# Performance work log

Measured on AMD Instinct MI355X. Metric: run time of the kernel, lower is better.

Reference implementation:

```python
import jax, jax.numpy as jnp
import numpy as np
from jax import lax
from jax.scipy.special import erf

SB, NV, NR = 2, 3, 2048
NC, NS, NG = 1000, 40, 15
H = W = 256
HID = 256
DEPTH_DIFF_MAX = 0.05
IMG = jnp.array([float(W), float(H)], dtype=jnp.float32)


def setup_inputs():
    key = jax.random.key(0)
    ks = jax.random.split(key, 10)
    origins = 0.1 * jax.random.normal(ks[0], (SB, NR, 3), jnp.float32)
    d_xy = 0.3 * jax.random.normal(ks[1], (SB, NR, 2), jnp.float32)
    dirs = jnp.concatenate([d_xy, jnp.ones((SB, NR, 1), jnp.float32)], -1)
    dirs = dirs / jnp.linalg.norm(dirs, axis=-1, keepdims=True)
    near = jnp.ones((SB, NR, 1), jnp.float32)
    far = 4.0 * jnp.ones((SB, NR, 1), jnp.float32)
    rays = jnp.concatenate([origins, dirs, near, far], -1)
    pose = jnp.eye(4, dtype=jnp.float32).at[2, 3].set(0.5)
    poses = jnp.broadcast_to(pose, (SB, NV, 4, 4))
    focal = 280.0 * jnp.ones((SB, NV, 2), jnp.float32)
    c = 128.0 * jnp.ones((SB, NV, 2), jnp.float32)
    depth_map = 1.5 + 3.0 * jax.random.uniform(ks[2], (SB, NV, 1, H, W), jnp.float32)
    depth_std_map = 0.01 + 0.2 * jax.random.uniform(ks[3], (SB, NV, 1, H, W), jnp.float32)
    nrm = jax.random.normal(ks[4], (SB, NV, 3, H, W), jnp.float32)
    normal_map = nrm / jnp.linalg.norm(nrm, axis=2, keepdims=True)
    W1 = 0.5 * jax.random.normal(ks[5], (6, HID), jnp.float32)
    b1 = jnp.zeros((HID,), jnp.float32)
    W2 = 0.1 * jax.random.normal(ks[6], (HID, 4), jnp.float32)
    b2 = jnp.zeros((4,), jnp.float32)
    u_coarse = jax.random.uniform(ks[7], (SB, NR, NC), jnp.float32)
    g_noise = jax.random.normal(ks[8], (SB, NR, NG), jnp.float32)
    u_fill = jax.random.uniform(ks[9], (SB, NR, NS), jnp.float32)
    return dict(rays=rays, poses=poses, focal=focal, c=c, depth_map=depth_map,
                depth_std_map=depth_std_map, normal_map=normal_map,
                W1=W1, b1=b1, W2=W2, b2=b2,
                u_coarse=u_coarse, g_noise=g_noise, u_fill=u_fill)


def _index_map(feat, uv):
    # feat: (SB,NV,C,H,W), uv: (SB,NV,P,2) in [-1,1] -> (SB,NV,C,P), nearest lookup
    sb, nv, ch, h, w = feat.shape
    x = jnp.clip(jnp.round((uv[..., 0] + 1) * 0.5 * w - 0.5), 0, w - 1).astype(jnp.int32)
    y = jnp.clip(jnp.round((uv[..., 1] + 1) * 0.5 * h - 0.5), 0, h - 1).astype(jnp.int32)
    lin = y * w + x
    flat = feat.reshape(sb, nv, ch, h * w)
    idx = jnp.broadcast_to(lin[:, :, None, :], (sb, nv, ch, lin.shape[-1]))
    return jnp.take_along_axis(flat, idx, axis=-1)


def _sample_z(rays, poses, focal, c, depth_map, depth_std_map, normal_map, u_coarse, g_noise, u_fill):
    near, far = rays[..., 6], rays[..., 7]
    step = 1.0 / NC
    # stratified coarse candidates (SB,NR,NC)
    z_steps = jnp.linspace(0.0, 1.0 - step, NC, dtype=jnp.float32)[None, None, :] + u_coarse * step
    z_cand = near[..., None] * (1 - z_steps) + far[..., None] * z_steps
    P = NR * NC
    xyz_w = (rays[..., None, :3] + z_cand[..., None] * rays[..., None, 3:6]).reshape(SB, P, 3)
    R, t = poses[:, :, :3, :3], poses[:, :, :3, 3]
    xyz = jnp.einsum('svij,spj->svpi', R, xyz_w) + t[:, :, None, :]   # (SB,NV,P,3) cam coords
    rdir_cam = jnp.einsum('svij,srj->svri', R, rays[..., 3:6])        # (SB,NV,NR,3)
    pdir_cam = jnp.repeat(rdir_cam, NC, axis=2)                        # (SB,NV,P,3)
    uv = xyz[..., :2] / xyz[..., 2:3]
    uv = (uv * focal[:, :, None, :] + c[:, :, None, :]) / IMG * 2 - 1
    ref_depth = _index_map(depth_map, uv)                              # (SB,NV,1,P)
    ref_std = _index_map(depth_std_map, uv)
    ref_normal = _index_map(normal_map, uv)                            # (SB,NV,3,P)
    ref_z = xyz[..., 2][:, :, None, :]                                 # (SB,NV,1,P)
    ss = jnp.repeat((far - near) / NC, NC, axis=1)[:, None, None, :]   # (SB,1,1,P)
    cosd = jnp.sum(jnp.swapaxes(pdir_cam, -2, -1) * ref_normal, axis=-2, keepdims=True)
    mask = (ref_std != 0) & (jnp.abs(ref_depth - ref_z) < DEPTH_DIFF_MAX) & (cosd <= 0)
    inv = 1.0 / (jnp.where(mask, ref_std, 1.0) * jnp.sqrt(2.0))
    lik = 0.5 * jnp.abs(erf((ref_z + ss / 2 - ref_depth) * inv) - erf((ref_z - ss / 2 - ref_depth) * inv))
    pt = jnp.where(mask, lik, 0.0)
    pt = jnp.max(pt, axis=1)[:, 0, :].reshape(SB, NR, NC)              # max over views
    opaque = jnp.concatenate(
        [pt[..., :1], pt[..., 1:] * jnp.cumprod(1.0 - pt, axis=-1)[..., :-1]], -1)
    sel_lik, idx = lax.top_k(pt, NS)                                   # descending shortlist
    z_sel = jnp.take_along_axis(z_cand, idx, axis=-1)
    z_sel = jnp.where(sel_lik == 0.0, 0.0, z_sel)
    # gaussian samples fitted to occlusion-aware likelihoods
    ray_mask = jnp.any(opaque != 0.0, axis=-1)                         # (SB,NR)
    wsum = jnp.sum(opaque, -1, keepdims=True)
    sw = jnp.where(wsum > 0, wsum, 1.0)
    mean = jnp.sum(z_cand * opaque, -1, keepdims=True) / sw
    std = jnp.sqrt(jnp.sum(opaque * (z_cand - mean) ** 2, -1, keepdims=True) / sw)
    gauss = jnp.where(ray_mask[..., None], g_noise * std + mean, 0.0)
    z_sel = z_sel.at[..., NS - NG:].set(gauss)
    # fill empty slots (zeros, which sort to the front) uniformly in [near, far]
    z = jnp.sort(z_sel, axis=-1)
    miss = z == 0.0
    n_miss = jnp.sum(miss, -1, keepdims=True)
    stepf = (far - near)[..., None] / jnp.maximum(n_miss, 1)
    z_fill = near[..., None] + jnp.arange(NS, dtype=jnp.float32)[None, None, :] * stepf + u_fill * stepf
    z = jnp.where(miss, z_fill, z)
    return jnp.sort(z, axis=-1)                                        # (SB,NR,NS)


def _composite(rays, z, W1, b1, W2, b2):
    deltas = jnp.concatenate([z[..., 1:] - z[..., :-1], rays[..., 7:8] - z[..., -1:]], -1)
    pts = rays[..., None, :3] + z[..., None] * rays[..., None, 3:6]    # (SB,NR,NS,3)
    dirs = jnp.broadcast_to(rays[..., None, 3:6], pts.shape)
    h = jax.nn.relu(jnp.concatenate([pts, dirs], -1) @ W1 + b1)        # NeRF surrogate MLP
    out = h @ W2 + b2                                                  # (SB,NR,NS,4)
    rgbs, sig = out[..., :3], out[..., 3]
    alphas = 1.0 - jnp.exp(-deltas * jax.nn.relu(sig))
    T = jnp.cumprod(jnp.concatenate([jnp.ones_like(alphas[..., :1]), 1.0 - alphas + 1e-10], -1), -1)
    weights = alphas * T[..., :-1]
    rgb = jnp.sum(weights[..., None] * rgbs, -2)
    depth = jnp.sum(weights * z, -1)
    rgb = rgb + 1.0 - jnp.sum(weights, -1, keepdims=True)              # white background
    return weights, rgb, depth


def reference(rays, poses, focal, c, depth_map, depth_std_map, normal_map, W1, b1, W2, b2, u_coarse, g_noise, u_fill):
    # depth-guided sampling is under @torch.no_grad in the original -> stop_gradient
    z = lax.stop_gradient(_sample_z(rays, poses, focal, c, depth_map, depth_std_map,
                                    normal_map, u_coarse, g_noise, u_fill))
    return _composite(rays, z, W1, b1, W2, b2)
```

## Files before the change

kernel.cpp:

```cpp
#include <hip/hip_runtime.h>
#include <math.h>

#define N_SB 2
#define N_V  3
#define N_R  2048
#define N_C  1000
#define N_S  40
#define N_G  15
#define N_HID 256
#define HW 65536
#define CAP 256

__device__ __forceinline__ float wave_sum(float v) {
#pragma unroll
  for (int off = 32; off > 0; off >>= 1) v += __shfl_xor(v, off);
  return v;
}

__device__ __forceinline__ float erf_xla(float x) {
  const float c = 3.832506856900711f;
  x = fminf(fmaxf(x, -c), c);
  float x2 = __fmul_rn(x, x);
  float p = 0.00022905065861350646f;
  p = __fadd_rn(__fmul_rn(p, x2), 0.0034082910107109506f);
  p = __fadd_rn(__fmul_rn(p, x2), 0.050955695062380861f);
  p = __fadd_rn(__fmul_rn(p, x2), 0.18520832239976145f);
  p = __fadd_rn(__fmul_rn(p, x2), 1.128379143519084f);
  float q = -1.1791602954361697e-7f;
  q = __fadd_rn(__fmul_rn(q, x2), 0.000023547966471313185f);
  q = __fadd_rn(__fmul_rn(q, x2), 0.0010179625278914885f);
  q = __fadd_rn(__fmul_rn(q, x2), 0.014070470171167667f);
  q = __fadd_rn(__fmul_rn(q, x2), 0.11098505178285362f);
  q = __fadd_rn(__fmul_rn(q, x2), 0.49746925110067538f);
  q = __fadd_rn(__fmul_rn(q, x2), 1.0f);
  return __fdiv_rn(__fmul_rn(x, p), q);
}

__device__ __forceinline__ float bitonic64(float v, int lane) {
#pragma unroll
  for (int k = 2; k <= 64; k <<= 1) {
#pragma unroll
    for (int j = k >> 1; j >= 1; j >>= 1) {
      float o = __shfl_xor(v, j);
      bool up = ((lane & k) == 0);
      bool lower = ((lane & j) == 0);
      v = (lower == up) ? fminf(v, o) : fmaxf(v, o);
    }
  }
  return v;
}

__global__ __launch_bounds__(256, 8)
void nerf_all(const float* __restrict__ rays, const float* __restrict__ poses,
              const float* __restrict__ focal, const float* __restrict__ cvec,
              const float* __restrict__ dmap, const float* __restrict__ smap,
              const float* __restrict__ nmap, const float* __restrict__ W1,
              const float* __restrict__ b1, const float* __restrict__ W2,
              const float* __restrict__ b2, const float* __restrict__ uc,
              const float* __restrict__ gn, const float* __restrict__ uf,
              float* __restrict__ out)
{
  __shared__ __align__(16) float s_pt[1024];
  __shared__ __align__(16) float s_zc[1024];
  __shared__ float s_lv[CAP];
  __shared__ int   s_li[CAP];
  __shared__ float s_lz[CAP];
  __shared__ int   s_cnt;
  __shared__ float s_cv[100];
  __shared__ int   s_ci[100];
  __shared__ float s_cz[100];
  __shared__ float s_zsel[32];
  __shared__ float s_wtot[4], s_sO[4], s_sZ[4], s_sV[4];
  __shared__ int   s_fl[4];
  __shared__ float s_zarr[N_S], s_darr[N_S];
  __shared__ float s_mlp[N_S * 4];

  const int tid = threadIdx.x;
  const int wid = tid >> 6;
  const int lane = tid & 63;
  const int ray = blockIdx.x;
  const int sb = ray >> 11;

  if (tid == 0) s_cnt = 0;
  if (tid < 100) { s_cv[tid] = 0.0f; s_ci[tid] = 0x40000000; s_cz[tid] = 0.0f; }
  if (tid < 32) s_zsel[tid] = 0.0f;

  const float* rp = rays + (size_t)ray * 8;
  const float ox = rp[0], oy = rp[1], oz = rp[2];
  const float dx = rp[3], dy = rp[4], dz = rp[5];
  const float nearv = rp[6], farv = rp[7];

  const float lindelta = 0.999f / 999.0f;
  const float ssv = __fdiv_rn(__fsub_rn(farv, nearv), 1000.0f);
  const float sshalf = __fmul_rn(ssv, 0.5f);
  const float SQRT2 = 1.41421356237309515f;

  float zg[4] = {0.0f, 0.0f, 0.0f, 0.0f};
  float ptg[4] = {0.0f, 0.0f, 0.0f, 0.0f};
#pragma unroll
  for (int cch = 0; cch < 4; ++cch) {
    const int i = cch * 256 + tid;
    if (i < N_C) {
      const float u = uc[(size_t)ray * N_C + i];
      const float zs = __fadd_rn(__fmul_rn((float)i, lindelta), __fmul_rn(u, 0.001f));
      const float zc = __fadd_rn(__fmul_rn(nearv, __fsub_rn(1.0f, zs)), __fmul_rn(farv, zs));
      zg[cch] = zc;
      s_zc[i] = zc;
    }
  }

#pragma unroll 1
  for (int v = 0; v < N_V; ++v) {
    const float* pp = poses + (size_t)(sb * N_V + v) * 16;
    const float R00 = pp[0], R01 = pp[1], R02 = pp[2], t0 = pp[3];
    const float R10 = pp[4], R11 = pp[5], R12 = pp[6], t1 = pp[7];
    const float R20 = pp[8], R21 = pp[9], R22 = pp[10], t2 = pp[11];
    const float fx = focal[(sb * N_V + v) * 2 + 0];
    const float fy = focal[(sb * N_V + v) * 2 + 1];
    const float cx = cvec[(sb * N_V + v) * 2 + 0];
    const float cy = cvec[(sb * N_V + v) * 2 + 1];
    const float rdx = __fadd_rn(__fadd_rn(__fmul_rn(R00, dx), __fmul_rn(R01, dy)), __fmul_rn(R02, dz));
    const float rdy = __fadd_rn(__fadd_rn(__fmul_rn(R10, dx), __fmul_rn(R11, dy)), __fmul_rn(R12, dz));
    const float rdz = __fadd_rn(__fadd_rn(__fmul_rn(R20, dx), __fmul_rn(R21, dy)), __fmul_rn(R22, dz));
    const float* dmv = dmap + (size_t)(sb * N_V + v) * HW;
    const float* smv = smap + (size_t)(sb * N_V + v) * HW;
    const float* nmv = nmap + (size_t)(sb * N_V + v) * 3 * HW;

    int   linv[4];
    float Zcv[4];
    float rdv[4];
#pragma unroll
    for (int cch = 0; cch < 4; ++cch) {
      const float zc = zg[cch];
      const float xw = __fadd_rn(ox, __fmul_rn(zc, dx));
      const float yw = __fadd_rn(oy, __fmul_rn(zc, dy));
      const float zw = __fadd_rn(oz, __fmul_rn(zc, dz));
      const float Xc = __fadd_rn(__fadd_rn(__fadd_rn(__fmul_rn(R00, xw), __fmul_rn(R01, yw)), __fmul_rn(R02, zw)), t0);
      const float Yc = __fadd_rn(__fadd_rn(__fadd_rn(__fmul_rn(R10, xw), __fmul_rn(R11, yw)), __fmul_rn(R12, zw)), t1);
      const float Zc = __fadd_rn(__fadd_rn(__fadd_rn(__fmul_rn(R20, xw), __fmul_rn(R21, yw)), __fmul_rn(R22, zw)), t2);
      const float iu = __fdiv_rn(Xc, Zc);
      const float iv = __fdiv_rn(Yc, Zc);
      const float su = __fadd_rn(__fmul_rn(iu, fx), cx);
      const float sv = __fadd_rn(__fmul_rn(iv, fy), cy);
      const float unorm = __fsub_rn(__fmul_rn(__fmul_rn(su, 1.0f / 256.0f), 2.0f), 1.0f);
      const float vnorm = __fsub_rn(__fmul_rn(__fmul_rn(sv, 1.0f / 256.0f), 2.0f), 1.0f);
      const float xf = __fsub_rn(__fmul_rn(__fmul_rn(__fadd_rn(unorm, 1.0f), 0.5f), 256.0f), 0.5f);
      const float yf = __fsub_rn(__fmul_rn(__fmul_rn(__fadd_rn(vnorm, 1.0f), 0.5f), 256.0f), 0.5f);
      const int px = (int)fminf(fmaxf(rintf(xf), 0.0f), 255.0f);
      const int py = (int)fminf(fmaxf(rintf(yf), 0.0f), 255.0f);
      linv[cch] = py * 256 + px;
      Zcv[cch] = Zc;
      rdv[cch] = dmv[linv[cch]];
    }

#pragma unroll
    for (int cch = 0; cch < 4; ++cch) {
      const int i = cch * 256 + tid;
      const float Zc = Zcv[cch];
      const float rd = rdv[cch];
      if (i < N_C && fabsf(__fsub_rn(rd, Zc)) < 0.05f) {
        const int lin = linv[cch];
        const float rs = smv[lin];
        const float n0 = nmv[lin];
        const float n1 = nmv[HW + lin];
        const float n2 = nmv[2 * HW + lin];
        const float cosd = __fadd_rn(__fadd_rn(__fmul_rn(rdx, n0), __fmul_rn(rdy, n1)), __fmul_rn(rdz, n2));
        if ((rs != 0.0f) && (cosd <= 0.0f)) {
          const float invv = __fdiv_rn(1.0f, __fmul_rn(rs, SQRT2));
          const float a1 = __fmul_rn(__fsub_rn(__fadd_rn(Zc, sshalf), rd), invv);
          const float a2 = __fmul_rn(__fsub_rn(__fsub_rn(Zc, sshalf), rd), invv);
          const float ptv = __fmul_rn(0.5f, fabsf(__fsub_rn(erf_xla(a1), erf_xla(a2))));
          ptg[cch] = fmaxf(ptg[cch], ptv);
        }
      }
    }
  }
#pragma unroll
  for (int cch = 0; cch < 4; ++cch) {
    const int i = cch * 256 + tid;
    if (i < N_C) s_pt[i] = ptg[cch];
  }
  __syncthreads();

  const bool act = (tid < 250);
  float ptm[4] = {0.0f, 0.0f, 0.0f, 0.0f};
  float zcr[4] = {0.0f, 0.0f, 0.0f, 0.0f};
  if (act) {
    const float4 p4 = *(const float4*)&s_pt[tid * 4];
    ptm[0] = p4.x; ptm[1] = p4.y; ptm[2] = p4.z; ptm[3] = p4.w;
    const float4 z4 = *(const float4*)&s_zc[tid * 4];
    zcr[0] = z4.x; zcr[1] = z4.y; zcr[2] = z4.z; zcr[3] = z4.w;
  }

  float lp = 1.0f;
  if (act) {
#pragma unroll
    for (int k = 0; k < 4; ++k) lp = __fmul_rn(lp, __fsub_rn(1.0f, ptm[k]));
  }
  float inc = lp;
#pragma unroll
  for (int off = 1; off < 64; off <<= 1) {
    float o = __shfl_up(inc, off);
    if (lane >= off) inc *= o;
  }
  if (lane == 63) s_wtot[wid] = inc;
  __syncthreads();
  float pw = 1.0f;
  if (wid > 0) pw *= s_wtot[0];
  if (wid > 1) pw *= s_wtot[1];
  if (wid > 2) pw *= s_wtot[2];
  float exc = __shfl_up(inc, 1);
  if (lane == 0) exc = 1.0f;
  exc *= pw;

  float accO = 0.0f, accZO = 0.0f;
  bool anynz = false;
  if (act) {
    float run = exc;
#pragma unroll
    for (int k = 0; k < 4; ++k) {
      float o = ptm[k] * run;
      accO += o;
      accZO += zcr[k] * o;
      anynz |= (o != 0.0f);
      run *= (1.0f - ptm[k]);
    }
  }
  accO = wave_sum(accO);
  accZO = wave_sum(accZO);
  const int anyw = __any(anynz) ? 1 : 0;
  if (lane == 0) { s_sO[wid] = accO; s_sZ[wid] = accZO; s_fl[wid] = anyw; }
  __syncthreads();
  const float tO = s_sO[0] + s_sO[1] + s_sO[2] + s_sO[3];
  const float tZ = s_sZ[0] + s_sZ[1] + s_sZ[2] + s_sZ[3];
  const bool raymask = (s_fl[0] | s_fl[1] | s_fl[2] | s_fl[3]) != 0;
  const float swd = (tO > 0.0f) ? tO : 1.0f;
  const float meanz = __fdiv_rn(tZ, swd);

  float accV = 0.0f;
  if (act) {
    float run = exc;
#pragma unroll
    for (int k = 0; k < 4; ++k) {
      float o = ptm[k] * run;
      float d = zcr[k] - meanz;
      accV += o * d * d;
      run *= (1.0f - ptm[k]);
    }
  }
  accV = wave_sum(accV);
  if (lane == 0) s_sV[wid] = accV;
  __syncthreads();
  const float tV = s_sV[0] + s_sV[1] + s_sV[2] + s_sV[3];
  const float stdz = sqrtf(__fdiv_rn(tV, swd));

  {
    const bool nz0 = act && (ptm[0] > 0.0f);
    const bool nz1 = act && (ptm[1] > 0.0f);
    const bool nz2 = act && (ptm[2] > 0.0f);
    const bool nz3 = act && (ptm[3] > 0.0f);
    const int nloc = (int)nz0 + (int)nz1 + (int)nz2 + (int)nz3;
    int base = 0;
    if (nloc > 0) base = atomicAdd(&s_cnt, nloc);
    if (base + nloc <= CAP) {
      int off = base;
      if (nz0) { s_lv[off] = ptm[0]; s_li[off] = tid * 4 + 0; s_lz[off] = zcr[0]; ++off; }
      if (nz1) { s_lv[off] = ptm[1]; s_li[off] = tid * 4 + 1; s_lz[off] = zcr[1]; ++off; }
      if (nz2) { s_lv[off] = ptm[2]; s_li[off] = tid * 4 + 2; s_lz[off] = zcr[2]; ++off; }
      if (nz3) { s_lv[off] = ptm[3]; s_li[off] = tid * 4 + 3; s_lz[off] = zcr[3]; ++off; }
    }
  }
  __syncthreads();
  const int cnt = s_cnt;

  if (cnt <= CAP) {
    if (wid == 0) {
      float rv[4]; int ri[4]; float rz[4];
#pragma unroll
      for (int j = 0; j < 4; ++j) {
        const int p = lane + j * 64;
        if (p < cnt) { rv[j] = s_lv[p]; ri[j] = s_li[p]; rz[j] = s_lz[p]; }
        else         { rv[j] = -2.0f; ri[j] = 0x40000000; rz[j] = 0.0f; }
      }
#pragma unroll 1
      for (int kk = 0; kk < 25; ++kk) {
        float bv = -2.0f; int bi = 0x40000000;
#pragma unroll
        for (int j = 0; j < 4; ++j) {
          if (rv[j] > bv || (rv[j] == bv && ri[j] < bi)) { bv = rv[j]; bi = ri[j]; }
        }
#pragma unroll
        for (int off = 1; off < 64; off <<= 1) {
          const float ov = __shfl_xor(bv, off);
          const int oi = __shfl_xor(bi, off);
          if (ov > bv || (ov == bv && oi < bi)) { bv = ov; bi = oi; }
        }
        if (bv <= 0.0f) break;
#pragma unroll
        for (int j = 0; j < 4; ++j) {
          if (ri[j] == bi) {
            s_zsel[kk] = rz[j];
            rv[j] = -1.0f;
          }
        }
      }
    }
  } else {
    const int cbase = wid * 25;
#pragma unroll 1
    for (int kk = 0; kk < 25; ++kk) {
      float bv = -2.0f;
      int bi = 0x40000000;
      if (act) {
#pragma unroll
        for (int k = 0; k < 4; ++k) {
          if (ptm[k] > bv) { bv = ptm[k]; bi = tid * 4 + k; }
        }
      }
#pragma unroll
      for (int off = 1; off < 64; off <<= 1) {
        float ov = __shfl_xor(bv, off);
        int oi = __shfl_xor(bi, off);
        if (ov > bv || (ov == bv && oi < bi)) { bv = ov; bi = oi; }
      }
      if (bv <= 0.0f) break;
      if (tid == (bi >> 2)) {
        s_cv[cbase + kk] = bv;
        s_ci[cbase + kk] = bi;
        const int r = bi & 3;
        float zk;
        if (r == 0)      { zk = zcr[0]; ptm[0] = -1.0f; }
        else if (r == 1) { zk = zcr[1]; ptm[1] = -1.0f; }
        else if (r == 2) { zk = zcr[2]; ptm[2] = -1.0f; }
        else             { zk = zcr[3]; ptm[3] = -1.0f; }
        s_cz[cbase + kk] = zk;
      }
    }
    __syncthreads();
    if (wid == 0) {
      float c0v = s_cv[lane];
      int   c0i = s_ci[lane];
      float c0z = s_cz[lane];
      float c1v = -2.0f; int c1i = 0x40000000; float c1z = 0.0f;
      if (lane + 64 < 100) { c1v = s_cv[lane + 64]; c1i = s_ci[lane + 64]; c1z = s_cz[lane + 64]; }
#pragma unroll 1
      for (int kk = 0; kk < 25; ++kk) {
        float bv = c0v; int bi = c0i; float bz = c0z;
        if (c1v > bv || (c1v == bv && c1i < bi)) { bv = c1v; bi = c1i; bz = c1z; }
#pragma unroll
        for (int off = 1; off < 64; off <<= 1) {
          float ov = __shfl_xor(bv, off);
          int oi = __shfl_xor(bi, off);
          float oz = __shfl_xor(bz, off);
          if (ov > bv || (ov == bv && oi < bi)) { bv = ov; bi = oi; bz = oz; }
        }
        if (bv <= 0.0f) break;
        if (lane == 0) s_zsel[kk] = bz;
        if (c0i == bi) c0v = -1.0f;
        if (c1i == bi) c1v = -1.0f;
      }
    }
  }

  if (wid == 0) {
    float sortv;
    if (lane < N_S - N_G) {
      sortv = s_zsel[lane];
    } else if (lane < N_S) {
      const float g = gn[(size_t)ray * N_G + (lane - (N_S - N_G))];
      sortv = raymask ? (g * stdz + meanz) : 0.0f;
    } else {
      sortv = INFINITY;
    }
    float z = bitonic64(sortv, lane);
    const bool miss = (lane < N_S) && (z == 0.0f);
    const int nmiss_raw = __popcll(__ballot(miss));
    const int nmiss = (nmiss_raw < 1) ? 1 : nmiss_raw;
    const float stepf = __fdiv_rn(__fsub_rn(farv, nearv), (float)nmiss);
    if (miss) {
      const float ufv = uf[(size_t)ray * N_S + lane];
      z = __fadd_rn(__fadd_rn(nearv, __fmul_rn((float)lane, stepf)), __fmul_rn(ufv, stepf));
    }
    z = bitonic64(z, lane);
    const float zn = __shfl_down(z, 1);
    const float delta = (lane == N_S - 1) ? (farv - z) : (zn - z);
    if (lane < N_S) { s_zarr[lane] = z; s_darr[lane] = delta; }
  }
  __syncthreads();

  {
    const float b2r = (lane < 4) ? b2[lane] : 0.0f;
    float w1r[24], b1r[4], w2r[16];
#pragma unroll
    for (int m = 0; m < 4; ++m) {
      const int j = lane + 64 * m;
#pragma unroll
      for (int k = 0; k < 6; ++k) w1r[k * 4 + m] = W1[k * N_HID + j];
      b1r[m] = b1[j];
      const float4 w2v = *(const float4*)(W2 + (size_t)j * 4);
      w2r[m * 4 + 0] = w2v.x; w2r[m * 4 + 1] = w2v.y;
      w2r[m * 4 + 2] = w2v.z; w2r[m * 4 + 3] = w2v.w;
    }
#pragma unroll 1
    for (int q = 0; q < 10; ++q) {
      const int s = wid * 10 + q;
      const float zq = s_zarr[s];
      const float px = ox + zq * dx;
      const float py = oy + zq * dy;
      const float pz = oz + zq * dz;
      float a0 = 0.0f, a1 = 0.0f, a2 = 0.0f, a3 = 0.0f;
#pragma unroll
      for (int m = 0; m < 4; ++m) {
        float h = b1r[m];
        h = fmaf(px, w1r[0 * 4 + m], h);
        h = fmaf(py, w1r[1 * 4 + m], h);
        h = fmaf(pz, w1r[2 * 4 + m], h);
        h = fmaf(dx, w1r[3 * 4 + m], h);
        h = fmaf(dy, w1r[4 * 4 + m], h);
        h = fmaf(dz, w1r[5 * 4 + m], h);
        h = fmaxf(h, 0.0f);
        a0 = fmaf(h, w2r[m * 4 + 0], a0);
        a1 = fmaf(h, w2r[m * 4 + 1], a1);
        a2 = fmaf(h, w2r[m * 4 + 2], a2);
        a3 = fmaf(h, w2r[m * 4 + 3], a3);
      }
      const float s0 = __shfl_xor(a0, 1), s1 = __shfl_xor(a1, 1);
      const float s2 = __shfl_xor(a2, 1), s3 = __shfl_xor(a3, 1);
      const float m0 = (lane & 1) ? (a1 + s1) : (a0 + s0);
      const float m1 = (lane & 1) ? (a3 + s3) : (a2 + s2);
      const float t0 = __shfl_xor(m0, 2), t1 = __shfl_xor(m1, 2);
      float r = (lane & 2) ? (m1 + t1) : (m0 + t0);
#pragma unroll
      for (int off = 4; off < 64; off <<= 1) r += __shfl_xor(r, off);
      if (lane < 4) s_mlp[s * 4 + lane] = r + b2r;
    }
  }
  __syncthreads();

  if (wid == 0) {
    float alpha = 0.0f, r0 = 0.0f, r1 = 0.0f, r2 = 0.0f, zl = 0.0f;
    float factor = 1.0f;
    if (lane < N_S) {
      zl = s_zarr[lane];
      const float dl = s_darr[lane];
      r0 = s_mlp[lane * 4 + 0];
      r1 = s_mlp[lane * 4 + 1];
      r2 = s_mlp[lane * 4 + 2];
      const float rsig = fmaxf(s_mlp[lane * 4 + 3], 0.0f);
      alpha = 1.0f - expf(-dl * rsig);
      factor = (1.0f - alpha) + 1e-10f;
    }
    float incp = factor;
#pragma unroll
    for (int off = 1; off < 64; off <<= 1) {
      float o = __shfl_up(incp, off);
      if (lane >= off) incp *= o;
    }
    float T = __shfl_up(incp, 1);
    if (lane == 0) T = 1.0f;

    const float w = (lane < N_S) ? alpha * T : 0.0f;
    const float wz = (lane < N_S) ? w * zl : 0.0f;
    const float wr0 = (lane < N_S) ? w * r0 : 0.0f;
    const float wr1 = (lane < N_S) ? w * r1 : 0.0f;
    const float wr2 = (lane < N_S) ? w * r2 : 0.0f;

    const float wsum = wave_sum(w);
    const float dsum = wave_sum(wz);
    const float c0s = wave_sum(wr0);
    const float c1s = wave_sum(wr1);
    const float c2s = wave_sum(wr2);

    if (lane < N_S) out[(size_t)ray * N_S + lane] = w;
    if (lane == 0) {
      float* rgbo = out + (size_t)N_SB * N_R * N_S + (size_t)ray * 3;
      rgbo[0] = (c0s + 1.0f) - wsum;
      rgbo[1] = (c1s + 1.0f) - wsum;
      rgbo[2] = (c2s + 1.0f) - wsum;
      out[(size_t)N_SB * N_R * N_S + (size_t)N_SB * N_R * 3 + ray] = dsum;
    }
  }
}

extern "C" void kernel_launch(void* const* d_in, const int* in_sizes, int n_in,
                              void* d_out, int out_size, void* d_ws, size_t ws_size,
                              hipStream_t stream) {
  const float* rays  = (const float*)d_in[0];
  const float* poses = (const float*)d_in[1];
  const float* focal = (const float*)d_in[2];
  const float* cvec  = (const float*)d_in[3];
  const float* dmap  = (const float*)d_in[4];
  const float* smap  = (const float*)d_in[5];
  const float* nmap  = (const float*)d_in[6];
  const float* W1p   = (const float*)d_in[7];
  const float* b1p   = (const float*)d_in[8];
  const float* W2p   = (const float*)d_in[9];
  const float* b2p   = (const float*)d_in[10];
  const float* ucp   = (const float*)d_in[11];
  const float* gnp   = (const float*)d_in[12];
  const float* ufp   = (const float*)d_in[13];
  float* outp = (float*)d_out;

  dim3 grid(N_SB * N_R);
  dim3 block(256);
  nerf_all<<<grid, block, 0, stream>>>(rays, poses, focal, cvec, dmap, smap, nmap,
                                       W1p, b1p, W2p, b2p, ucp, gnp, ufp, outp);
}
```

Before: 96.59 us.

## Cut register pressure: union shared buffers, pair projections, split MLP hidden across waves

Several scattered shared arrays are merged into one aliased buffer, so the MLP partial sums reuse the space of dead sampling arrays. Coarse z values now live in LDS rather than registers, and the projection and gating run two samples at a time through helper functions. The MLP is reorganised so each thread owns one hidden unit across all 40 samples instead of four units for 10 samples. Per-wave partial results are reduced by wave 0 from LDS. The goal is to lower register and LDS footprint for higher occupancy, at the cost of extra LDS reads and a changed summation order.

Measured after the change: 141.3 us. +46.3%, slower.

```diff
diff --git a/kernel.cpp b/kernel.cpp
--- a/kernel.cpp
+++ b/kernel.cpp
@@ -7,7 +7,6 @@
 #define N_C  1000
 #define N_S  40
 #define N_G  15
-#define N_HID 256
 #define HW 65536
 #define CAP 256
 
@@ -50,6 +49,57 @@
   return v;
 }
 
+__device__ __forceinline__ void proj_one(
+    float zc, float ox, float oy, float oz, float dx, float dy, float dz,
+    float R00, float R01, float R02, float t0,
+    float R10, float R11, float R12, float t1,
+    float R20, float R21, float R22, float t2,
+    float fx, float fy, float cx, float cy,
+    int& lin_out, float& Zc_out)
+{
+  const float xw = __fadd_rn(ox, __fmul_rn(zc, dx));
+  const float yw = __fadd_rn(oy, __fmul_rn(zc, dy));
+  const float zw = __fadd_rn(oz, __fmul_rn(zc, dz));
+  const float Xc = __fadd_rn(__fadd_rn(__fadd_rn(__fmul_rn(R00, xw), __fmul_rn(R01, yw)), __fmul_rn(R02, zw)), t0);
+  const float Yc = __fadd_rn(__fadd_rn(__fadd_rn(__fmul_rn(R10, xw), __fmul_rn(R11, yw)), __fmul_rn(R12, zw)), t1);
+  const float Zc = __fadd_rn(__fadd_rn(__fadd_rn(__fmul_rn(R20, xw), __fmul_rn(R21, yw)), __fmul_rn(R22, zw)), t2);
+  const float iu = __fdiv_rn(Xc, Zc);
+  const float iv = __fdiv_rn(Yc, Zc);
+  const float su = __fadd_rn(__fmul_rn(iu, fx), cx);
+  const float sv = __fadd_rn(__fmul_rn(iv, fy), cy);
+  const float unorm = __fsub_rn(__fmul_rn(__fmul_rn(su, 1.0f / 256.0f), 2.0f), 1.0f);
+  const float vnorm = __fsub_rn(__fmul_rn(__fmul_rn(sv, 1.0f / 256.0f), 2.0f), 1.0f);
+  const float xf = __fsub_rn(__fmul_rn(__fmul_rn(__fadd_rn(unorm, 1.0f), 0.5f), 256.0f), 0.5f);
+  const float yf = __fsub_rn(__fmul_rn(__fmul_rn(__fadd_rn(vnorm, 1.0f), 0.5f), 256.0f), 0.5f);
+  const int px = (int)fminf(fmaxf(rintf(xf), 0.0f), 255.0f);
+  const int py = (int)fminf(fmaxf(rintf(yf), 0.0f), 255.0f);
+  lin_out = py * 256 + px;
+  Zc_out = Zc;
+}
+
+__device__ __forceinline__ float gate_one(
+    int i, int lin, float Zc, float rd,
+    const float* __restrict__ smv, const float* __restrict__ nmv,
+    float rdx, float rdy, float rdz, float sshalf, float cur)
+{
+  const float SQRT2 = 1.41421356237309515f;
+  if (i < N_C && fabsf(__fsub_rn(rd, Zc)) < 0.05f) {
+    const float rs = smv[lin];
+    const float n0 = nmv[lin];
+    const float n1 = nmv[HW + lin];
+    const float n2 = nmv[2 * HW + lin];
+    const float cosd = __fadd_rn(__fadd_rn(__fmul_rn(rdx, n0), __fmul_rn(rdy, n1)), __fmul_rn(rdz, n2));
+    if ((rs != 0.0f) && (cosd <= 0.0f)) {
+      const float invv = __fdiv_rn(1.0f, __fmul_rn(rs, SQRT2));
+      const float a1 = __fmul_rn(__fsub_rn(__fadd_rn(Zc, sshalf), rd), invv);
+      const float a2 = __fmul_rn(__fsub_rn(__fsub_rn(Zc, sshalf), rd), invv);
+      const float ptv = __fmul_rn(0.5f, fabsf(__fsub_rn(erf_xla(a1), erf_xla(a2))));
+      cur = fmaxf(cur, ptv);
+    }
+  }
+  return cur;
+}
+
 __global__ __launch_bounds__(256, 8)
 void nerf_all(const float* __restrict__ rays, const float* __restrict__ poses,
               const float* __restrict__ focal, const float* __restrict__ cvec,
@@ -60,20 +110,22 @@
               const float* __restrict__ gn, const float* __restrict__ uf,
               float* __restrict__ out)
 {
-  __shared__ __align__(16) float s_pt[1024];
-  __shared__ __align__(16) float s_zc[1024];
-  __shared__ float s_lv[CAP];
-  __shared__ int   s_li[CAP];
-  __shared__ float s_lz[CAP];
+  __shared__ __align__(16) float s_buf[3120];
   __shared__ int   s_cnt;
-  __shared__ float s_cv[100];
-  __shared__ int   s_ci[100];
-  __shared__ float s_cz[100];
   __shared__ float s_zsel[32];
   __shared__ float s_wtot[4], s_sO[4], s_sZ[4], s_sV[4];
   __shared__ int   s_fl[4];
   __shared__ float s_zarr[N_S], s_darr[N_S];
-  __shared__ float s_mlp[N_S * 4];
+
+  float* const s_pt = s_buf;
+  float* const s_zc = s_buf + 1024;
+  float* const s_lv = s_buf + 2048;
+  int*   const s_li = (int*)(s_buf + 2304);
+  float* const s_lz = s_buf + 2560;
+  float* const s_cv = s_buf + 2816;
+  int*   const s_ci = (int*)(s_buf + 2916);
+  float* const s_cz = s_buf + 3016;
+  float* const s_pp = s_buf;
 
   const int tid = threadIdx.x;
   const int wid = tid >> 6;
@@ -93,22 +145,20 @@
   const float lindelta = 0.999f / 999.0f;
   const float ssv = __fdiv_rn(__fsub_rn(farv, nearv), 1000.0f);
   const float sshalf = __fmul_rn(ssv, 0.5f);
-  const float SQRT2 = 1.41421356237309515f;
-
-  float zg[4] = {0.0f, 0.0f, 0.0f, 0.0f};
-  float ptg[4] = {0.0f, 0.0f, 0.0f, 0.0f};
+
 #pragma unroll
   for (int cch = 0; cch < 4; ++cch) {
     const int i = cch * 256 + tid;
     if (i < N_C) {
       const float u = uc[(size_t)ray * N_C + i];
       const float zs = __fadd_rn(__fmul_rn((float)i, lindelta), __fmul_rn(u, 0.001f));
-      const float zc = __fadd_rn(__fmul_rn(nearv, __fsub_rn(1.0f, zs)), __fmul_rn(farv, zs));
-      zg[cch] = zc;
-      s_zc[i] = zc;
-    }
-  }
-
+      s_zc[i] = __fadd_rn(__fmul_rn(nearv, __fsub_rn(1.0f, zs)), __fmul_rn(farv, zs));
+    } else {
+      s_zc[i] = 0.0f;
+    }
+  }
+
+  float ptg0 = 0.0f, ptg1 = 0.0f, ptg2 = 0.0f, ptg3 = 0.0f;
 #pragma unroll 1
   for (int v = 0; v < N_V; ++v) {
     const float* pp = poses + (size_t)(sb * N_V + v) * 16;
@@ -126,60 +176,37 @@
     const float* smv = smap + (size_t)(sb * N_V + v) * HW;
     const float* nmv = nmap + (size_t)(sb * N_V + v) * 3 * HW;
 
-    int   linv[4];
-    float Zcv[4];
-    float rdv[4];
-#pragma unroll
-    for (int cch = 0; cch < 4; ++cch) {
-      const float zc = zg[cch];
-      const float xw = __fadd_rn(ox, __fmul_rn(zc, dx));
-      const float yw = __fadd_rn(oy, __fmul_rn(zc, dy));
-      const float zw = __fadd_rn(oz, __fmul_rn(zc, dz));
-      const float Xc = __fadd_rn(__fadd_rn(__fadd_rn(__fmul_rn(R00, xw), __fmul_rn(R01, yw)), __fmul_rn(R02, zw)), t0);
-      const float Yc = __fadd_rn(__fadd_rn(__fadd_rn(__fmul_rn(R10, xw), __fmul_rn(R11, yw)), __fmul_rn(R12, zw)), t1);
-      const float Zc = __fadd_rn(__fadd_rn(__fadd_rn(__fmul_rn(R20, xw), __fmul_rn(R21, yw)), __fmul_rn(R22, zw)), t2);
-      const float iu = __fdiv_rn(Xc, Zc);
-      const float iv = __fdiv_rn(Yc, Zc);
-      const float su = __fadd_rn(__fmul_rn(iu, fx), cx);
-      const float sv = __fadd_rn(__fmul_rn(iv, fy), cy);
-      const float unorm = __fsub_rn(__fmul_rn(__fmul_rn(su, 1.0f / 256.0f), 2.0f), 1.0f);
-      const float vnorm = __fsub_rn(__fmul_rn(__fmul_rn(sv, 1.0f / 256.0f), 2.0f), 1.0f);
-      const float xf = __fsub_rn(__fmul_rn(__fmul_rn(__fadd_rn(unorm, 1.0f), 0.5f), 256.0f), 0.5f);
-      const float yf = __fsub_rn(__fmul_rn(__fmul_rn(__fadd_rn(vnorm, 1.0f), 0.5f), 256.0f), 0.5f);
-      const int px = (int)fminf(fmaxf(rintf(xf), 0.0f), 255.0f);
-      const int py = (int)fminf(fmaxf(rintf(yf), 0.0f), 255.0f);
-      linv[cch] = py * 256 + px;
-      Zcv[cch] = Zc;
-      rdv[cch] = dmv[linv[cch]];
-    }
-
-#pragma unroll
-    for (int cch = 0; cch < 4; ++cch) {
-      const int i = cch * 256 + tid;
-      const float Zc = Zcv[cch];
-      const float rd = rdv[cch];
-      if (i < N_C && fabsf(__fsub_rn(rd, Zc)) < 0.05f) {
-        const int lin = linv[cch];
-        const float rs = smv[lin];
-        const float n0 = nmv[lin];
-        const float n1 = nmv[HW + lin];
-        const float n2 = nmv[2 * HW + lin];
-        const float cosd = __fadd_rn(__fadd_rn(__fmul_rn(rdx, n0), __fmul_rn(rdy, n1)), __fmul_rn(rdz, n2));
-        if ((rs != 0.0f) && (cosd <= 0.0f)) {
-          const float invv = __fdiv_rn(1.0f, __fmul_rn(rs, SQRT2));
-          const float a1 = __fmul_rn(__fsub_rn(__fadd_rn(Zc, sshalf), rd), invv);
-          const float a2 = __fmul_rn(__fsub_rn(__fsub_rn(Zc, sshalf), rd), invv);
-          const float ptv = __fmul_rn(0.5f, fabsf(__fsub_rn(erf_xla(a1), erf_xla(a2))));
-          ptg[cch] = fmaxf(ptg[cch], ptv);
-        }
-      }
-    }
-  }
-#pragma unroll
-  for (int cch = 0; cch < 4; ++cch) {
-    const int i = cch * 256 + tid;
-    if (i < N_C) s_pt[i] = ptg[cch];
-  }
+    {
+      int lin0, lin1; float Zc0, Zc1;
+      proj_one(s_zc[tid], ox, oy, oz, dx, dy, dz,
+               R00, R01, R02, t0, R10, R11, R12, t1, R20, R21, R22, t2,
+               fx, fy, cx, cy, lin0, Zc0);
+      proj_one(s_zc[256 + tid], ox, oy, oz, dx, dy, dz,
+               R00, R01, R02, t0, R10, R11, R12, t1, R20, R21, R22, t2,
+               fx, fy, cx, cy, lin1, Zc1);
+      const float rd0 = dmv[lin0];
+      const float rd1 = dmv[lin1];
+      ptg0 = gate_one(tid,       lin0, Zc0, rd0, smv, nmv, rdx, rdy, rdz, sshalf, ptg0);
+      ptg1 = gate_one(256 + tid, lin1, Zc1, rd1, smv, nmv, rdx, rdy, rdz, sshalf, ptg1);
+    }
+    {
+      int lin2, lin3; float Zc2, Zc3;
+      proj_one(s_zc[512 + tid], ox, oy, oz, dx, dy, dz,
+               R00, R01, R02, t0, R10, R11, R12, t1, R20, R21, R22, t2,
+               fx, fy, cx, cy, lin2, Zc2);
+      proj_one(s_zc[768 + tid], ox, oy, oz, dx, dy, dz,
+               R00, R01, R02, t0, R10, R11, R12, t1, R20, R21, R22, t2,
+               fx, fy, cx, cy, lin3, Zc3);
+      const float rd2 = dmv[lin2];
+      const float rd3 = dmv[lin3];
+      ptg2 = gate_one(512 + tid, lin2, Zc2, rd2, smv, nmv, rdx, rdy, rdz, sshalf, ptg2);
+      ptg3 = gate_one(768 + tid, lin3, Zc3, rd3, smv, nmv, rdx, rdy, rdz, sshalf, ptg3);
+    }
+  }
+  s_pt[tid] = ptg0;
+  s_pt[256 + tid] = ptg1;
+  s_pt[512 + tid] = ptg2;
+  if (768 + tid < N_C) s_pt[768 + tid] = ptg3;
   __syncthreads();
 
   const bool act = (tid < 250);
@@ -389,41 +416,30 @@
   __syncthreads();
 
   {
-    const float b2r = (lane < 4) ? b2[lane] : 0.0f;
-    float w1r[24], b1r[4], w2r[16];
-#pragma unroll
-    for (int m = 0; m < 4; ++m) {
-      const int j = lane + 64 * m;
-#pragma unroll
-      for (int k = 0; k < 6; ++k) w1r[k * 4 + m] = W1[k * N_HID + j];
-      b1r[m] = b1[j];
-      const float4 w2v = *(const float4*)(W2 + (size_t)j * 4);
-      w2r[m * 4 + 0] = w2v.x; w2r[m * 4 + 1] = w2v.y;
-      w2r[m * 4 + 2] = w2v.z; w2r[m * 4 + 3] = w2v.w;
-    }
+    const int j = tid;
+    const float w10 = W1[0 * 256 + j];
+    const float w11 = W1[1 * 256 + j];
+    const float w12 = W1[2 * 256 + j];
+    const float w13 = W1[3 * 256 + j];
+    const float w14 = W1[4 * 256 + j];
+    const float w15 = W1[5 * 256 + j];
+    const float b1j = b1[j];
+    const float4 w2j = *(const float4*)(W2 + (size_t)j * 4);
 #pragma unroll 1
-    for (int q = 0; q < 10; ++q) {
-      const int s = wid * 10 + q;
+    for (int s = 0; s < N_S; ++s) {
       const float zq = s_zarr[s];
       const float px = ox + zq * dx;
       const float py = oy + zq * dy;
       const float pz = oz + zq * dz;
-      float a0 = 0.0f, a1 = 0.0f, a2 = 0.0f, a3 = 0.0f;
-#pragma unroll
-      for (int m = 0; m < 4; ++m) {
-        float h = b1r[m];
-        h = fmaf(px, w1r[0 * 4 + m], h);
-        h = fmaf(py, w1r[1 * 4 + m], h);
-        h = fmaf(pz, w1r[2 * 4 + m], h);
-        h = fmaf(dx, w1r[3 * 4 + m], h);
-        h = fmaf(dy, w1r[4 * 4 + m], h);
-        h = fmaf(dz, w1r[5 * 4 + m], h);
-        h = fmaxf(h, 0.0f);
-        a0 = fmaf(h, w2r[m * 4 + 0], a0);
-        a1 = fmaf(h, w2r[m * 4 + 1], a1);
-        a2 = fmaf(h, w2r[m * 4 + 2], a2);
-        a3 = fmaf(h, w2r[m * 4 + 3], a3);
-      }
+      float h = b1j;
+      h = fmaf(px, w10, h);
+      h = fmaf(py, w11, h);
+      h = fmaf(pz, w12, h);
+      h = fmaf(dx, w13, h);
+      h = fmaf(dy, w14, h);
+      h = fmaf(dz, w15, h);
+      h = fmaxf(h, 0.0f);
+      float a0 = h * w2j.x, a1 = h * w2j.y, a2 = h * w2j.z, a3 = h * w2j.w;
       const float s0 = __shfl_xor(a0, 1), s1 = __shfl_xor(a1, 1);
       const float s2 = __shfl_xor(a2, 1), s3 = __shfl_xor(a3, 1);
       const float m0 = (lane & 1) ? (a1 + s1) : (a0 + s0);
@@ -432,7 +448,7 @@
       float r = (lane & 2) ? (m1 + t1) : (m0 + t0);
 #pragma unroll
       for (int off = 4; off < 64; off <<= 1) r += __shfl_xor(r, off);
-      if (lane < 4) s_mlp[s * 4 + lane] = r + b2r;
+      if (lane < 4) s_pp[s * 16 + lane * 4 + wid] = r;
     }
   }
   __syncthreads();
@@ -443,10 +459,15 @@
     if (lane < N_S) {
       zl = s_zarr[lane];
       const float dl = s_darr[lane];
-      r0 = s_mlp[lane * 4 + 0];
-      r1 = s_mlp[lane * 4 + 1];
-      r2 = s_mlp[lane * 4 + 2];
-      const float rsig = fmaxf(s_mlp[lane * 4 + 3], 0.0f);
+      const float4 q0 = *(const float4*)&s_pp[lane * 16 + 0];
+      const float4 q1 = *(const float4*)&s_pp[lane * 16 + 4];
+      const float4 q2 = *(const float4*)&s_pp[lane * 16 + 8];
+      const float4 q3 = *(const float4*)&s_pp[lane * 16 + 12];
+      r0 = (((q0.x + q0.y) + q0.z) + q0.w) + b2[0];
+      r1 = (((q1.x + q1.y) + q1.z) + q1.w) + b2[1];
+      r2 = (((q2.x + q2.y) + q2.z) + q2.w) + b2[2];
+      const float sig = (((q3.x + q3.y) + q3.z) + q3.w) + b2[3];
+      const float rsig = fmaxf(sig, 0.0f);
       alpha = 1.0f - expf(-dl * rsig);
       factor = (1.0f - alpha) + 1e-10f;
     }
```
